# Kernel tuning notes

Hardware: AMD Instinct MI355X
Metric: run time of the kernel (lower is better)

## Reference

```python
import jax, jax.numpy as jnp
import numpy as np

E = 1024  # embed_dim
H = 1     # num_heads (energy_W matmul forces head_dim == embed_dim)
TEMPERATURE = 1.0


def setup_inputs() -> dict:
    key = jax.random.key(0)
    ks = jax.random.split(key, 10)
    B, S = 8, 2048
    inp = {
        "query": jax.random.normal(ks[0], (B, S, E), dtype=jnp.float32),
        "key": jax.random.normal(ks[1], (B, S, E), dtype=jnp.float32),
        "value": jax.random.normal(ks[2], (B, S, E), dtype=jnp.float32),
        "mask": jnp.ones((1, 1, S, S), dtype=jnp.int32),
        # nn.Linear params (y = x @ W.T + b)
        "Wq": jax.random.normal(ks[3], (E, E), dtype=jnp.float32) * (1.0 / np.sqrt(E)),
        "bq": jnp.zeros((E,), dtype=jnp.float32),
        "Wk": jax.random.normal(ks[4], (E, E), dtype=jnp.float32) * (1.0 / np.sqrt(E)),
        "bk": jnp.zeros((E,), dtype=jnp.float32),
        "Wv": jax.random.normal(ks[5], (E, E), dtype=jnp.float32) * (1.0 / np.sqrt(E)),
        "bv": jnp.zeros((E,), dtype=jnp.float32),
        "energy_W": jax.random.normal(ks[6], (E, E), dtype=jnp.float32),
    }
    return inp


def reference(query, key, value, mask, Wq, bq, Wk, bk, Wv, bv, energy_W):
    B, S, _ = query.shape
    hd = E // H
    # projections (torch Linear: x @ W.T + b), then split heads -> [B, H, S, hd]
    q = (query @ Wq.T + bq).reshape(B, S, H, hd).transpose(0, 2, 1, 3)
    k = (key @ Wk.T + bk).reshape(B, S, H, hd).transpose(0, 2, 1, 3)
    v = (value @ Wv.T + bv).reshape(B, S, H, hd).transpose(0, 2, 1, 3)
    # bilinear energy: (q) @ (k @ W)^T   -> [B, H, Sq, Sk]
    k_t = k @ energy_W
    energy = jnp.einsum("bhqd,bhkd->bhqk", q, k_t) / TEMPERATURE
    energy = jnp.where(mask == 0, jnp.float32(-1e9), energy)
    attn_weights = jax.nn.softmax(-energy, axis=-1)
    out = jnp.einsum("bhqk,bhkd->bhqd", attn_weights, v)
    out = out.transpose(0, 2, 1, 3).reshape(B, S, E)
    return (out, attn_weights)
```

## Files before the change

kernel.cpp:

```cpp
#include <hip/hip_runtime.h>


typedef __attribute__((ext_vector_type(8))) short short8;
typedef __attribute__((ext_vector_type(4))) float f32x4;

#define E_DIM 1024
#define S_LEN 2048
#define NB 8

__device__ __forceinline__ unsigned short rne_bf(float x) {
    unsigned int u = __float_as_uint(x);
    return (unsigned short)((u + 0x7fffu + ((u >> 16) & 1u)) >> 16);
}

__device__ __forceinline__ void splitbf(float x, unsigned short& h, unsigned short& l) {
    unsigned int u = __float_as_uint(x);
    unsigned int rh = ((u + 0x7fffu + ((u >> 16) & 1u)) >> 16) << 16;
    h = (unsigned short)(rh >> 16);
    float r = x - __uint_as_float(rh);
    unsigned int v = __float_as_uint(r);
    l = (unsigned short)((v + 0x7fffu + ((v >> 16) & 1u)) >> 16);
}

__device__ __forceinline__ void lds_cp16(const void* g, void* l) {
    __builtin_amdgcn_global_load_lds(
        (const __attribute__((address_space(1))) unsigned int*)g,
        (__attribute__((address_space(3))) unsigned int*)l, 16, 0, 0);
}

__device__ __forceinline__ void wait_vm8() { asm volatile("s_waitcnt vmcnt(8)" ::: "memory"); }
__device__ __forceinline__ void wait_vm4() { asm volatile("s_waitcnt vmcnt(4)" ::: "memory"); }
__device__ __forceinline__ void wait_vm0() { asm volatile("s_waitcnt vmcnt(0)" ::: "memory"); }

template <bool DO_L>
__global__ __launch_bounds__(256) void conv_img(
    const float* __restrict__ src, unsigned short* __restrict__ h,
    unsigned short* __restrict__ l, int ld, int nkt)
{
    const int t = threadIdx.x;
    const long long tb = ((long long)blockIdx.y * nkt + blockIdx.x) * 4096;
    const float* s0 = src + (long long)blockIdx.y * 128 * ld + blockIdx.x * 32;
#pragma unroll
    for (int i = 0; i < 4; ++i) {
        const int f = i * 256 + t;
        const int r = f >> 3;
        const int c4 = (f & 7) << 2;
        const float4 v = *(const float4*)(s0 + (long long)r * ld + c4);
        const int gg = c4 >> 3;
        const int half = (c4 >> 2) & 1;
        const long long wo = tb + (long long)(gg * 128 + r) * 8 + half * 4;
        unsigned short h0, h1, h2, h3;
        if (DO_L) {
            unsigned short l0, l1, l2, l3;
            splitbf(v.x, h0, l0); splitbf(v.y, h1, l1);
            splitbf(v.z, h2, l2); splitbf(v.w, h3, l3);
            uint2 hp, lp;
            hp.x = h0 | ((unsigned)h1 << 16); hp.y = h2 | ((unsigned)h3 << 16);
            lp.x = l0 | ((unsigned)l1 << 16); lp.y = l2 | ((unsigned)l3 << 16);
            *(uint2*)(h + wo) = hp;
            *(uint2*)(l + wo) = lp;
        } else {
            h0 = rne_bf(v.x); h1 = rne_bf(v.y); h2 = rne_bf(v.z); h3 = rne_bf(v.w);
            uint2 hp;
            hp.x = h0 | ((unsigned)h1 << 16); hp.y = h2 | ((unsigned)h3 << 16);
            *(uint2*)(h + wo) = hp;
        }
    }
}

template <int NPROD, int WMODE>
__global__ __launch_bounds__(256) void gemm_img(
    const unsigned short* __restrict__ Ah, const unsigned short* __restrict__ Al,
    const unsigned short* __restrict__ Bh, const unsigned short* __restrict__ Bl,
    float* __restrict__ C, const float* __restrict__ bias,
    unsigned short* __restrict__ imgH, unsigned short* __restrict__ imgL,
    int ldC, long long bsC, int nkt, int aZrb, int bZrb, int outNkt)
{
    extern __shared__ unsigned short sm[];

    const int t = threadIdx.x;
    const int wv = t >> 6, lane = t & 63;
    const int wm = (wv >> 1) << 6, wn = (wv & 1) << 6;
    const int lr = lane & 15, gq = lane >> 4;

    int bx = blockIdx.x, by = blockIdx.y;
    {
        const int gx = gridDim.x, nwg = gx * gridDim.y;
        if ((nwg & 7) == 0) {
            const int w = by * gx + bx;
            const int cpx = nwg >> 3;
            const int sw = (w & 7) * cpx + (w >> 3);
            bx = sw % gx;
            by = sw / gx;
        }
    }

    const long long aB0 = ((long long)blockIdx.z * aZrb + by) * nkt * 4096;
    const long long bB0 = ((long long)blockIdx.z * bZrb + bx) * nkt * 4096;

    auto srcptr = [&](int s, const unsigned short*& aS, const unsigned short*& bS) {
        int seg, kt;
        if (NPROD == 3) {
            seg = (s >= 2 * nkt) ? 2 : (s >= nkt ? 1 : 0);
            kt = s - seg * nkt;
        } else { seg = 0; kt = s; }
        aS = ((NPROD == 3 && seg == 1) ? Al : Ah) + aB0 + (long long)kt * 4096;
        bS = ((NPROD == 3 && seg == 2) ? Bl : Bh) + bB0 + (long long)kt * 4096;
    };
    auto stage = [&](const unsigned short* aS, const unsigned short* bS, int c) {
        unsigned short* dA = sm + c * 8192;
        unsigned short* dB = dA + 4096;
#pragma unroll
        for (int j = 0; j < 2; ++j) {
            lds_cp16(aS + (wv * 128 + j * 64 + lane) * 8, dA + (wv * 128 + j * 64) * 8);
            lds_cp16(bS + (wv * 128 + j * 64 + lane) * 8, dB + (wv * 128 + j * 64) * 8);
        }
    };

    f32x4 acc[4][4] = {};
    const int nsteps = NPROD * nkt;

    {
        const unsigned short *aS, *bS;
        srcptr(0, aS, bS); stage(aS, bS, 0);
        srcptr(1, aS, bS); stage(aS, bS, 1);
    }

    int cur = 0;
    for (int s = 0; s < nsteps; ++s) {
        __builtin_amdgcn_s_barrier();
        if (s + 2 < nsteps) {
            const unsigned short *aS, *bS;
            srcptr(s + 2, aS, bS);
            stage(aS, bS, (cur + 2) % 3);
        }
        if (s + 2 < nsteps) wait_vm8();
        else if (s + 1 < nsteps) wait_vm4();
        else wait_vm0();
        __builtin_amdgcn_s_barrier();
        __builtin_amdgcn_sched_barrier(0);

        const unsigned short* smA = sm + cur * 8192;
        const unsigned short* smB = smA + 4096;
        short8 af[4], bfr[4];
        const unsigned short* pa = smA + (gq * 128 + wm + lr) * 8;
        const unsigned short* pb = smB + (gq * 128 + wn + lr) * 8;
#pragma unroll
        for (int m = 0; m < 4; ++m) af[m] = *(const short8*)(pa + m * 128);
#pragma unroll
        for (int n = 0; n < 4; ++n) bfr[n] = *(const short8*)(pb + n * 128);
        __builtin_amdgcn_s_setprio(1);
#pragma unroll
        for (int m = 0; m < 4; ++m)
#pragma unroll
            for (int n = 0; n < 4; ++n)
                acc[m][n] = __builtin_amdgcn_mfma_f32_16x16x32_bf16(af[m], bfr[n], acc[m][n], 0, 0, 0);
        __builtin_amdgcn_s_setprio(0);
        cur = (cur + 1) % 3;
    }

    const int cr = (lane >> 4) << 2, cc = lane & 15;
    if (WMODE == 0) {
        float* Cb = C + (long long)blockIdx.z * bsC;
#pragma unroll
        for (int m = 0; m < 4; ++m)
#pragma unroll
            for (int n = 0; n < 4; ++n) {
                const int gc = bx * 128 + wn + n * 16 + cc;
                const float badd = bias ? bias[gc] : 0.0f;
                const int gr0 = by * 128 + wm + m * 16 + cr;
#pragma unroll
                for (int i = 0; i < 4; ++i)
                    Cb[(long long)(gr0 + i) * ldC + gc] = acc[m][n][i] + badd;
            }
    } else {
        float* slab = (float*)sm;
        const int wmi = wv >> 1;
#pragma unroll
        for (int m = 0; m < 4; ++m) {
            __syncthreads();
#pragma unroll
            for (int n = 0; n < 4; ++n) {
                const int col = wn + n * 16 + cc;
                const float badd = bias ? bias[bx * 128 + col] : 0.0f;
#pragma unroll
                for (int i = 0; i < 4; ++i)
                    slab[(wmi * 16 + cr + i) * 132 + col] = acc[m][n][i] + badd;
            }
            __syncthreads();
            if (WMODE == 1) {
#pragma unroll
                for (int it = 0; it < 2; ++it) {
                    const int e = it * 256 + t;
                    const int wq = e >> 8, cg = (e >> 4) & 15, fr = e & 15;
                    const float* sp = slab + (wq * 16 + fr) * 132 + cg * 8;
                    const int rIn = wq * 64 + m * 16 + fr;
                    const int ktO = bx * 4 + (cg >> 2);
                    const int gO = cg & 3;
                    const long long base =
                        ((long long)by * outNkt + ktO) * 4096 + (gO * 128 + rIn) * 8;
                    unsigned short h[8], l[8];
#pragma unroll
                    for (int j = 0; j < 8; ++j) splitbf(sp[j], h[j], l[j]);
                    uint4 hp, lp;
                    hp.x = h[0] | ((unsigned)h[1] << 16); hp.y = h[2] | ((unsigned)h[3] << 16);
                    hp.z = h[4] | ((unsigned)h[5] << 16); hp.w = h[6] | ((unsigned)h[7] << 16);
                    lp.x = l[0] | ((unsigned)l[1] << 16); lp.y = l[2] | ((unsigned)l[3] << 16);
                    lp.z = l[4] | ((unsigned)l[5] << 16); lp.w = l[6] | ((unsigned)l[7] << 16);
                    *(uint4*)(imgH + base) = hp;
                    *(uint4*)(imgL + base) = lp;
                }
            } else {
#pragma unroll
                for (int it = 0; it < 2; ++it) {
                    const int e = it * 256 + t;
                    const int wq = e >> 8, s8 = (e >> 7) & 1, dl = e & 127;
                    const int sG = by * 128 + wq * 64 + m * 16 + s8 * 8;
                    const int z = sG >> 11, sIn = sG & 2047;
                    const int ktO = sIn >> 5, gO = (sIn >> 3) & 3;
                    const long long base =
                        ((long long)(z * 8 + bx) * 64 + ktO) * 4096 + (gO * 128 + dl) * 8;
                    unsigned short h[8];
#pragma unroll
                    for (int j = 0; j < 8; ++j)
                        h[j] = rne_bf(slab[(wq * 16 + s8 * 8 + j) * 132 + dl]);
                    uint4 hp;
                    hp.x = h[0] | ((unsigned)h[1] << 16); hp.y = h[2] | ((unsigned)h[3] << 16);
                    hp.z = h[4] | ((unsigned)h[5] << 16); hp.w = h[6] | ((unsigned)h[7] << 16);
                    *(uint4*)(imgH + base) = hp;
                }
            }
        }
    }
}

__global__ __launch_bounds__(256) void softmax_img(
    float* __restrict__ attn, const int* __restrict__ mask,
    unsigned short* __restrict__ img)
{
    const int row = blockIdx.x;
    const int q = row & (S_LEN - 1);
    const int t = threadIdx.x;
    const int lane = t & 63, wid = t >> 6;
    float* rp = attn + (long long)row * S_LEN;
    const int* mp = mask + (long long)q * S_LEN;

    const float4 e0 = *(const float4*)(rp + t * 8);
    const float4 e1 = *(const float4*)(rp + t * 8 + 4);
    const int4 ma = *(const int4*)(mp + t * 8);
    const int4 mb = *(const int4*)(mp + t * 8 + 4);
    float zv[8];
    zv[0] = ma.x ? -e0.x : 1e9f;
    zv[1] = ma.y ? -e0.y : 1e9f;
    zv[2] = ma.z ? -e0.z : 1e9f;
    zv[3] = ma.w ? -e0.w : 1e9f;
    zv[4] = mb.x ? -e1.x : 1e9f;
    zv[5] = mb.y ? -e1.y : 1e9f;
    zv[6] = mb.z ? -e1.z : 1e9f;
    zv[7] = mb.w ? -e1.w : 1e9f;
    float mx = zv[0];
#pragma unroll
    for (int j = 1; j < 8; ++j) mx = fmaxf(mx, zv[j]);
#pragma unroll
    for (int o = 32; o > 0; o >>= 1) mx = fmaxf(mx, __shfl_xor(mx, o));
    __shared__ float redm[4], reds[4];
    if (lane == 0) redm[wid] = mx;
    __syncthreads();
    mx = fmaxf(fmaxf(redm[0], redm[1]), fmaxf(redm[2], redm[3]));
    float s = 0.f;
#pragma unroll
    for (int j = 0; j < 8; ++j) { zv[j] = expf(zv[j] - mx); s += zv[j]; }
#pragma unroll
    for (int o = 32; o > 0; o >>= 1) s += __shfl_xor(s, o);
    if (lane == 0) reds[wid] = s;
    __syncthreads();
    s = reds[0] + reds[1] + reds[2] + reds[3];
    const float inv = 1.0f / s;
    float4 o0, o1;
    o0.x = zv[0] * inv; o0.y = zv[1] * inv; o0.z = zv[2] * inv; o0.w = zv[3] * inv;
    o1.x = zv[4] * inv; o1.y = zv[5] * inv; o1.z = zv[6] * inv; o1.w = zv[7] * inv;
    *(float4*)(rp + t * 8) = o0;
    *(float4*)(rp + t * 8 + 4) = o1;
    const int z = row >> 11, rb = (row >> 7) & 15;
    const int ktO = t >> 2, gO = t & 3, r = row & 127;
    const long long base = (((long long)(z * 16 + rb) * 64 + ktO) * 512 + gO * 128 + r) * 8;
    uint4 hp;
    hp.x = rne_bf(o0.x) | ((unsigned)rne_bf(o0.y) << 16);
    hp.y = rne_bf(o0.z) | ((unsigned)rne_bf(o0.w) << 16);
    hp.z = rne_bf(o1.x) | ((unsigned)rne_bf(o1.y) << 16);
    hp.w = rne_bf(o1.z) | ((unsigned)rne_bf(o1.w) << 16);
    *(uint4*)(img + base) = hp;
}

__global__ void transpose1024(const float* __restrict__ in, float* __restrict__ out)
{
    __shared__ float tile[32][33];
    const int bx = blockIdx.x << 5, by = blockIdx.y << 5;
    const int tx = threadIdx.x, ty = threadIdx.y;
#pragma unroll
    for (int i = 0; i < 4; ++i)
        tile[ty + 8 * i][tx] = in[(long long)(by + ty + 8 * i) * E_DIM + bx + tx];
    __syncthreads();
#pragma unroll
    for (int i = 0; i < 4; ++i)
        out[(long long)(bx + ty + 8 * i) * E_DIM + by + tx] = tile[tx][ty + 8 * i];
}

__global__ __launch_bounds__(256) void bias_c_kernel(
    const float* __restrict__ We, const float* __restrict__ bq, float* __restrict__ c)
{
    const int i = blockIdx.x;
    const int t = threadIdx.x;
    float s = 0.f;
    for (int d = t; d < E_DIM; d += 256) s += bq[d] * We[(long long)i * E_DIM + d];
#pragma unroll
    for (int o = 32; o > 0; o >>= 1) s += __shfl_xor(s, o);
    __shared__ float red[4];
    if ((t & 63) == 0) red[t >> 6] = s;
    __syncthreads();
    if (t == 0) c[i] = red[0] + red[1] + red[2] + red[3];
}

template <bool SPLIT, int WMODE>
__global__ __launch_bounds__(256) void gemm_split(
    const float* __restrict__ A, const float* __restrict__ B,
    float* __restrict__ C, const float* __restrict__ bias,
    int M, int N, int K,
    long long bsA, long long bsB, long long bsC)
{
    extern __shared__ unsigned short sm[];
    unsigned short* sAh = sm;
    unsigned short* sBh = sm + 5120;
    unsigned short* sAl = sm + 10240;
    unsigned short* sBl = sm + 15360;

    const int t = threadIdx.x;
    const int z = blockIdx.z;
    const float* Ab = A + (long long)z * bsA + (long long)blockIdx.y * 128 * K;
    const float* Bb = B + (long long)z * bsB + (long long)blockIdx.x * 128 * K;

    const int wv = t >> 6;
    const int lane = t & 63;
    const int wm = (wv >> 1) << 6;
    const int wn = (wv & 1) << 6;
    const int lr = lane & 15;
    const int ko = (lane >> 4) << 3;

    f32x4 acc[4][4] = {};

    for (int k0 = 0; k0 < K; k0 += 32) {
        __syncthreads();
#pragma unroll
        for (int i = 0; i < 4; ++i) {
            const int f = t + (i << 8);
            const int row = f >> 3;
            const int c4 = (f & 7) << 2;
            const float4 av = *(const float4*)(Ab + (long long)row * K + k0 + c4);
            const float4 bv = *(const float4*)(Bb + (long long)row * K + k0 + c4);
            if (SPLIT) {
                unsigned short h0, h1, h2, h3, l0, l1, l2, l3;
                splitbf(av.x, h0, l0); splitbf(av.y, h1, l1);
                splitbf(av.z, h2, l2); splitbf(av.w, h3, l3);
                uint2 hp, lp;
                hp.x = (unsigned)h0 | ((unsigned)h1 << 16);
                hp.y = (unsigned)h2 | ((unsigned)h3 << 16);
                lp.x = (unsigned)l0 | ((unsigned)l1 << 16);
                lp.y = (unsigned)l2 | ((unsigned)l3 << 16);
                *(uint2*)(sAh + row * 40 + c4) = hp;
                *(uint2*)(sAl + row * 40 + c4) = lp;
                splitbf(bv.x, h0, l0); splitbf(bv.y, h1, l1);
                splitbf(bv.z, h2, l2); splitbf(bv.w, h3, l3);
                hp.x = (unsigned)h0 | ((unsigned)h1 << 16);
                hp.y = (unsigned)h2 | ((unsigned)h3 << 16);
                lp.x = (unsigned)l0 | ((unsigned)l1 << 16);
                lp.y = (unsigned)l2 | ((unsigned)l3 << 16);
                *(uint2*)(sBh + row * 40 + c4) = hp;
                *(uint2*)(sBl + row * 40 + c4) = lp;
            } else {
                uint2 hp;
                hp.x = (unsigned)rne_bf(av.x) | ((unsigned)rne_bf(av.y) << 16);
                hp.y = (unsigned)rne_bf(av.z) | ((unsigned)rne_bf(av.w) << 16);
                *(uint2*)(sAh + row * 40 + c4) = hp;
                hp.x = (unsigned)rne_bf(bv.x) | ((unsigned)rne_bf(bv.y) << 16);
                hp.y = (unsigned)rne_bf(bv.z) | ((unsigned)rne_bf(bv.w) << 16);
                *(uint2*)(sBh + row * 40 + c4) = hp;
            }
        }
        __syncthreads();
        short8 ah[4], bh[4], al[4], bl[4];
#pragma unroll
        for (int m = 0; m < 4; ++m)
            ah[m] = *(const short8*)(sAh + (wm + m * 16 + lr) * 40 + ko);
#pragma unroll
        for (int n = 0; n < 4; ++n)
            bh[n] = *(const short8*)(sBh + (wn + n * 16 + lr) * 40 + ko);
        if (SPLIT) {
#pragma unroll
            for (int m = 0; m < 4; ++m)
                al[m] = *(const short8*)(sAl + (wm + m * 16 + lr) * 40 + ko);
#pragma unroll
            for (int n = 0; n < 4; ++n)
                bl[n] = *(const short8*)(sBl + (wn + n * 16 + lr) * 40 + ko);
        }
#pragma unroll
        for (int m = 0; m < 4; ++m) {
#pragma unroll
            for (int n = 0; n < 4; ++n) {
                acc[m][n] = __builtin_amdgcn_mfma_f32_16x16x32_bf16(ah[m], bh[n], acc[m][n], 0, 0, 0);
                if (SPLIT) {
                    acc[m][n] = __builtin_amdgcn_mfma_f32_16x16x32_bf16(ah[m], bl[n], acc[m][n], 0, 0, 0);
                    acc[m][n] = __builtin_amdgcn_mfma_f32_16x16x32_bf16(al[m], bh[n], acc[m][n], 0, 0, 0);
                }
            }
        }
    }

    const int cr = (lane >> 4) << 2;
    const int cc = lane & 15;
    float* Cb = C + (long long)z * bsC;
#pragma unroll
    for (int m = 0; m < 4; ++m) {
#pragma unroll
        for (int n = 0; n < 4; ++n) {
            const int gc = blockIdx.x * 128 + wn + n * 16 + cc;
            const float badd = bias ? bias[gc] : 0.0f;
            const int gr0 = blockIdx.y * 128 + wm + m * 16 + cr;
#pragma unroll
            for (int i = 0; i < 4; ++i) {
                const float val = acc[m][n][i] + badd;
                if (WMODE == 0) {
                    Cb[(long long)(gr0 + i) * N + gc] = val;
                } else {
                    const int r = gr0 + i;
                    Cb[(long long)(r >> 11) * ((long long)N * 2048) +
                       (long long)gc * 2048 + (r & 2047)] = val;
                }
            }
        }
    }
}

__global__ __launch_bounds__(256) void softmax_rows(
    float* __restrict__ attn, const int* __restrict__ mask)
{
    const int row = blockIdx.x;
    const int q = row & (S_LEN - 1);
    const int t = threadIdx.x;
    const int lane = t & 63, wid = t >> 6;
    float* rp = attn + (long long)row * S_LEN;
    const int* mp = mask + (long long)q * S_LEN;

    float zv[8];
    float mx = -3.4e38f;
#pragma unroll
    for (int j = 0; j < 8; ++j) {
        const int idx = t + (j << 8);
        const float e = rp[idx];
        const int mv = mp[idx];
        const float zz = (mv != 0) ? -e : 1e9f;
        zv[j] = zz;
        mx = fmaxf(mx, zz);
    }
#pragma unroll
    for (int o = 32; o > 0; o >>= 1) mx = fmaxf(mx, __shfl_xor(mx, o));
    __shared__ float redm[4], reds[4];
    if (lane == 0) redm[wid] = mx;
    __syncthreads();
    mx = fmaxf(fmaxf(redm[0], redm[1]), fmaxf(redm[2], redm[3]));

    float s = 0.f;
#pragma unroll
    for (int j = 0; j < 8; ++j) { zv[j] = expf(zv[j] - mx); s += zv[j]; }
#pragma unroll
    for (int o = 32; o > 0; o >>= 1) s += __shfl_xor(s, o);
    if (lane == 0) reds[wid] = s;
    __syncthreads();
    s = reds[0] + reds[1] + reds[2] + reds[3];
    const float inv = 1.0f / s;
#pragma unroll
    for (int j = 0; j < 8; ++j) rp[t + (j << 8)] = zv[j] * inv;
}

extern "C" void kernel_launch(void* const* d_in, const int* in_sizes, int n_in,
                              void* d_out, int out_size, void* d_ws, size_t ws_size,
                              hipStream_t stream)
{
    const float* query = (const float*)d_in[0];
    const float* key   = (const float*)d_in[1];
    const float* value = (const float*)d_in[2];
    const int*   mask  = (const int*)d_in[3];
    const float* Wq    = (const float*)d_in[4];
    const float* bq    = (const float*)d_in[5];
    const float* Wk    = (const float*)d_in[6];
    const float* bk    = (const float*)d_in[7];
    const float* Wv    = (const float*)d_in[8];
    const float* bv    = (const float*)d_in[9];
    const float* We    = (const float*)d_in[10];

    float* out  = (float*)d_out;
    float* attn = out + (long long)NB * S_LEN * E_DIM;

    const size_t oWqT  = 0;
    const size_t oCvec = oWqT + (4u << 20);
    const size_t oWqTH = oCvec + 4096;
    const size_t oWqTL = oWqTH + (2u << 20);
    const size_t oWeH  = oWqTL + (2u << 20);
    const size_t oWeL  = oWeH + (2u << 20);
    const size_t oWkH  = oWeL + (2u << 20);
    const size_t oWkL  = oWkH + (2u << 20);
    const size_t oWvH  = oWkL + (2u << 20);
    const size_t oPH   = oWvH + (2u << 20);
    const size_t oPL   = oPH + (2u << 20);
    const size_t oBig1 = oPL + (2u << 20);
    const size_t oBig2 = oBig1 + (64u << 20);
    const size_t oBig3 = oBig2 + (64u << 20);
    const size_t NEED  = oBig3 + (64u << 20);

    char* wsb = (char*)d_ws;

    if (ws_size >= NEED) {
        float* WqT  = (float*)(wsb + oWqT);
        float* cvec = (float*)(wsb + oCvec);
        unsigned short* WqTH = (unsigned short*)(wsb + oWqTH);
        unsigned short* WqTL = (unsigned short*)(wsb + oWqTL);
        unsigned short* WeH  = (unsigned short*)(wsb + oWeH);
        unsigned short* WeL  = (unsigned short*)(wsb + oWeL);
        unsigned short* WkH  = (unsigned short*)(wsb + oWkH);
        unsigned short* WkL  = (unsigned short*)(wsb + oWkL);
        unsigned short* WvH  = (unsigned short*)(wsb + oWvH);
        unsigned short* PH   = (unsigned short*)(wsb + oPH);
        unsigned short* PL   = (unsigned short*)(wsb + oPL);
        unsigned short* qryH = (unsigned short*)(wsb + oBig1);
        unsigned short* qryL = (unsigned short*)(wsb + oBig1 + (32u << 20));
        unsigned short* attnH = (unsigned short*)(wsb + oBig1);
        unsigned short* keyH = (unsigned short*)(wsb + oBig2);
        unsigned short* keyL = (unsigned short*)(wsb + oBig2 + (32u << 20));
        unsigned short* qwH  = (unsigned short*)(wsb + oBig2);
        unsigned short* qwL  = (unsigned short*)(wsb + oBig2 + (32u << 20));
        unsigned short* kH   = (unsigned short*)(wsb + oBig3);
        unsigned short* kL   = (unsigned short*)(wsb + oBig3 + (32u << 20));
        unsigned short* vTH  = (unsigned short*)(wsb + oBig3);
        unsigned short* valH = (unsigned short*)(wsb + oBig3 + (32u << 20));

        transpose1024<<<dim3(32, 32), dim3(32, 8), 0, stream>>>(Wq, WqT);
        bias_c_kernel<<<1024, 256, 0, stream>>>(We, bq, cvec);
        conv_img<true><<<dim3(32, 8), 256, 0, stream>>>(WqT, WqTH, WqTL, 1024, 32);
        conv_img<true><<<dim3(32, 8), 256, 0, stream>>>(We, WeH, WeL, 1024, 32);
        conv_img<true><<<dim3(32, 8), 256, 0, stream>>>(Wk, WkH, WkL, 1024, 32);
        conv_img<false><<<dim3(32, 8), 256, 0, stream>>>(Wv, WvH, nullptr, 1024, 32);
        conv_img<true><<<dim3(32, 128), 256, 0, stream>>>(query, qryH, qryL, 1024, 32);
        conv_img<true><<<dim3(32, 128), 256, 0, stream>>>(key, keyH, keyL, 1024, 32);

        gemm_img<3, 1><<<dim3(8, 8, 1), 256, 49152, stream>>>(
            WeH, WeL, WqTH, WqTL, nullptr, nullptr, PH, PL, 0, 0, 32, 0, 0, 32);
        gemm_img<3, 1><<<dim3(8, 128, 1), 256, 49152, stream>>>(
            keyH, keyL, WkH, WkL, nullptr, bk, kH, kL, 0, 0, 32, 0, 0, 32);
        gemm_img<3, 1><<<dim3(8, 128, 1), 256, 49152, stream>>>(
            qryH, qryL, PH, PL, nullptr, cvec, qwH, qwL, 0, 0, 32, 0, 0, 32);
        gemm_img<3, 0><<<dim3(16, 16, NB), 256, 49152, stream>>>(
            qwH, qwL, kH, kL, attn, nullptr, nullptr, nullptr,
            2048, (long long)S_LEN * S_LEN, 32, 16, 16, 0);
        conv_img<false><<<dim3(32, 128), 256, 0, stream>>>(value, valH, nullptr, 1024, 32);
        gemm_img<1, 3><<<dim3(8, 128, 1), 256, 49152, stream>>>(
            valH, nullptr, WvH, nullptr, nullptr, bv, vTH, nullptr, 0, 0, 32, 0, 0, 0);
        softmax_img<<<NB * S_LEN, 256, 0, stream>>>(attn, mask, attnH);
        gemm_img<1, 0><<<dim3(8, 16, NB), 256, 49152, stream>>>(
            attnH, nullptr, vTH, nullptr, out, nullptr, nullptr, nullptr,
            1024, (long long)S_LEN * E_DIM, 64, 16, 8, 0);
    } else {
        float* ws   = (float*)d_ws;
        float* WqT  = ws;
        float* P    = WqT + 1048576;
        float* cvec = P + 1048576;
        float* kbuf = cvec + 1024;
        float* qw   = kbuf + 16777216;
        float* vT   = qw + 16777216;
        const size_t need_old = (size_t)(1048576 * 2 + 1024 + 16777216 * 3) * 4;
        if (ws_size < need_old) return;

        transpose1024<<<dim3(32, 32), dim3(32, 8), 0, stream>>>(Wq, WqT);
        bias_c_kernel<<<1024, 256, 0, stream>>>(We, bq, cvec);
        gemm_split<true, 0><<<dim3(8, 8, 1), 256, 40960, stream>>>(
            We, WqT, P, nullptr, 1024, 1024, 1024, 0, 0, 0);
        gemm_split<true, 0><<<dim3(8, 128, 1), 256, 40960, stream>>>(
            key, Wk, kbuf, bk, 16384, 1024, 1024, 0, 0, 0);
        gemm_split<false, 1><<<dim3(8, 128, 1), 256, 20480, stream>>>(
            value, Wv, vT, bv, 16384, 1024, 1024, 0, 0, 0);
        gemm_split<true, 0><<<dim3(8, 128, 1), 256, 40960, stream>>>(
            query, P, qw, cvec, 16384, 1024, 1024, 0, 0, 0);
        gemm_split<true, 0><<<dim3(16, 16, NB), 256, 40960, stream>>>(
            qw, kbuf, attn, nullptr, 2048, 2048, 1024,
            (long long)S_LEN * E_DIM, (long long)S_LEN * E_DIM, (long long)S_LEN * S_LEN);
        softmax_rows<<<NB * S_LEN, 256, 0, stream>>>(attn, mask);
        gemm_split<false, 0><<<dim3(8, 16, NB), 256, 20480, stream>>>(
            attn, vT, out, nullptr, 2048, 1024, 2048,
            (long long)S_LEN * S_LEN, (long long)E_DIM * S_LEN, (long long)S_LEN * E_DIM);
    }

    (void)in_sizes; (void)n_in; (void)out_size;
}
```

Baseline: 824.3 us.

## Add 256x128-tile 512-thread GEMM kernel for energy and output matmuls

Introduces gemm_big, a 512-thread kernel that computes a 256x128 output tile per block with a three-stage LDS ring buffered by direct global-to-LDS loads, and uses it for the QK^T energy GEMM and the attention-times-V GEMM. It also replaces the block remapping with a swizzle that groups blocks into 4x4 chunks per XCD to improve L2 reuse, applied to the existing GEMMs too. The larger tile halves the A/B refetch per output and the deeper pipeline aims to hide load latency. The cost is more registers and LDS per block, which may reduce occupancy.

```diff
diff --git a/kernel.cpp b/kernel.cpp
--- a/kernel.cpp
+++ b/kernel.cpp
@@ -29,8 +29,30 @@
 }
 
 __device__ __forceinline__ void wait_vm8() { asm volatile("s_waitcnt vmcnt(8)" ::: "memory"); }
+__device__ __forceinline__ void wait_vm6() { asm volatile("s_waitcnt vmcnt(6)" ::: "memory"); }
 __device__ __forceinline__ void wait_vm4() { asm volatile("s_waitcnt vmcnt(4)" ::: "memory"); }
+__device__ __forceinline__ void wait_vm3() { asm volatile("s_waitcnt vmcnt(3)" ::: "memory"); }
 __device__ __forceinline__ void wait_vm0() { asm volatile("s_waitcnt vmcnt(0)" ::: "memory"); }
+
+__device__ __forceinline__ void swizzle_xy(int& bx, int& by) {
+    const int gx = gridDim.x, gy = gridDim.y;
+    const int nwg = gx * gy;
+    const int w = by * gx + bx;
+    if ((gx & 3) == 0 && (gy & 3) == 0 && (((gx >> 2) * (gy >> 2)) & 7) == 0) {
+        const int nchx = gx >> 2;
+        const int xcd = w & 7, i = w >> 3;
+        const int j = i >> 4, p = i & 15;
+        const int ch = xcd + 8 * j;
+        const int chy = ch / nchx, chx = ch - chy * nchx;
+        by = chy * 4 + (p >> 2);
+        bx = chx * 4 + (p & 3);
+    } else if ((nwg & 7) == 0) {
+        const int cpx = nwg >> 3;
+        const int sw = (w & 7) * cpx + (w >> 3);
+        bx = sw % gx;
+        by = sw / gx;
+    }
+}
 
 template <bool DO_L>
 __global__ __launch_bounds__(256) void conv_img(
@@ -68,6 +90,109 @@
     }
 }
 
+template <int NPROD>
+__global__ __launch_bounds__(512, 4) void gemm_big(
+    const unsigned short* __restrict__ Ah, const unsigned short* __restrict__ Al,
+    const unsigned short* __restrict__ Bh, const unsigned short* __restrict__ Bl,
+    float* __restrict__ C, const float* __restrict__ bias,
+    int ldC, long long bsC, int nkt, int aZrb, int bZrb)
+{
+    __shared__ unsigned short smb[36864];
+
+    const int t = threadIdx.x;
+    const int wv = t >> 6, lane = t & 63;
+    const int wr = wv >> 1, wc = wv & 1;
+    const int lr = lane & 15, gq = lane >> 4;
+
+    int bx = blockIdx.x, by = blockIdx.y;
+    swizzle_xy(bx, by);
+
+    const long long aB0 = ((long long)blockIdx.z * aZrb + 2 * by) * nkt * 4096;
+    const long long aB1 = aB0 + (long long)nkt * 4096;
+    const long long bB0 = ((long long)blockIdx.z * bZrb + bx) * nkt * 4096;
+
+    auto srcptr = [&](int s, const unsigned short*& a0, const unsigned short*& a1,
+                      const unsigned short*& bS) {
+        int seg, kt;
+        if (NPROD == 3) {
+            seg = (s >= 2 * nkt) ? 2 : (s >= nkt ? 1 : 0);
+            kt = s - seg * nkt;
+        } else { seg = 0; kt = s; }
+        const unsigned short* aBase = ((NPROD == 3 && seg == 1) ? Al : Ah);
+        const unsigned short* bBase = ((NPROD == 3 && seg == 2) ? Bl : Bh);
+        a0 = aBase + aB0 + (long long)kt * 4096;
+        a1 = aBase + aB1 + (long long)kt * 4096;
+        bS = bBase + bB0 + (long long)kt * 4096;
+    };
+    auto stage = [&](const unsigned short* a0, const unsigned short* a1,
+                     const unsigned short* bS, int c) {
+        unsigned short* dA = smb + c * 12288;
+        lds_cp16(a0 + t * 8, dA + t * 8);
+        lds_cp16(a1 + t * 8, dA + 4096 + t * 8);
+        lds_cp16(bS + t * 8, dA + 8192 + t * 8);
+    };
+
+    f32x4 acc[4][4] = {};
+    const int nsteps = NPROD * nkt;
+
+    {
+        const unsigned short *a0, *a1, *bS;
+        srcptr(0, a0, a1, bS); stage(a0, a1, bS, 0);
+        srcptr(1, a0, a1, bS); stage(a0, a1, bS, 1);
+    }
+
+    int cur = 0;
+    for (int s = 0; s < nsteps; ++s) {
+        __builtin_amdgcn_s_barrier();
+        if (s + 2 < nsteps) {
+            const unsigned short *a0, *a1, *bS;
+            srcptr(s + 2, a0, a1, bS);
+            stage(a0, a1, bS, (cur + 2) % 3);
+        }
+        if (s + 2 < nsteps) wait_vm6();
+        else if (s + 1 < nsteps) wait_vm3();
+        else wait_vm0();
+        __builtin_amdgcn_s_barrier();
+        __builtin_amdgcn_sched_barrier(0);
+
+        const unsigned short* dA = smb + cur * 12288;
+        const unsigned short* dB = dA + 8192;
+        short8 af[4], bfr[4];
+#pragma unroll
+        for (int m = 0; m < 4; ++m) {
+            const int R = wr * 64 + m * 16 + lr;
+            af[m] = *(const short8*)(dA + (R >> 7) * 4096 + (gq * 128 + (R & 127)) * 8);
+        }
+#pragma unroll
+        for (int n = 0; n < 4; ++n) {
+            const int Cc = wc * 64 + n * 16 + lr;
+            bfr[n] = *(const short8*)(dB + (gq * 128 + Cc) * 8);
+        }
+        __builtin_amdgcn_s_setprio(1);
+#pragma unroll
+        for (int m = 0; m < 4; ++m)
+#pragma unroll
+            for (int n = 0; n < 4; ++n)
+                acc[m][n] = __builtin_amdgcn_mfma_f32_16x16x32_bf16(af[m], bfr[n], acc[m][n], 0, 0, 0);
+        __builtin_amdgcn_s_setprio(0);
+        cur = (cur + 1) % 3;
+    }
+
+    const int cr = (lane >> 4) << 2, cc = lane & 15;
+    float* Cb = C + (long long)blockIdx.z * bsC;
+#pragma unroll
+    for (int m = 0; m < 4; ++m)
+#pragma unroll
+        for (int n = 0; n < 4; ++n) {
+            const int gc = bx * 128 + wc * 64 + n * 16 + cc;
+            const float badd = bias ? bias[gc] : 0.0f;
+            const int gr0 = by * 256 + wr * 64 + m * 16 + cr;
+#pragma unroll
+            for (int i = 0; i < 4; ++i)
+                Cb[(long long)(gr0 + i) * ldC + gc] = acc[m][n][i] + badd;
+        }
+}
+
 template <int NPROD, int WMODE>
 __global__ __launch_bounds__(256) void gemm_img(
     const unsigned short* __restrict__ Ah, const unsigned short* __restrict__ Al,
@@ -84,16 +209,7 @@
     const int lr = lane & 15, gq = lane >> 4;
 
     int bx = blockIdx.x, by = blockIdx.y;
-    {
-        const int gx = gridDim.x, nwg = gx * gridDim.y;
-        if ((nwg & 7) == 0) {
-            const int w = by * gx + bx;
-            const int cpx = nwg >> 3;
-            const int sw = (w & 7) * cpx + (w >> 3);
-            bx = sw % gx;
-            by = sw / gx;
-        }
-    }
+    swizzle_xy(bx, by);
 
     const long long aB0 = ((long long)blockIdx.z * aZrb + by) * nkt * 4096;
     const long long bB0 = ((long long)blockIdx.z * bZrb + bx) * nkt * 4096;
@@ -557,16 +673,16 @@
             keyH, keyL, WkH, WkL, nullptr, bk, kH, kL, 0, 0, 32, 0, 0, 32);
         gemm_img<3, 1><<<dim3(8, 128, 1), 256, 49152, stream>>>(
             qryH, qryL, PH, PL, nullptr, cvec, qwH, qwL, 0, 0, 32, 0, 0, 32);
-        gemm_img<3, 0><<<dim3(16, 16, NB), 256, 49152, stream>>>(
-            qwH, qwL, kH, kL, attn, nullptr, nullptr, nullptr,
-            2048, (long long)S_LEN * S_LEN, 32, 16, 16, 0);
+        gemm_big<3><<<dim3(16, 8, NB), 512, 0, stream>>>(
+            qwH, qwL, kH, kL, attn, nullptr,
+            2048, (long long)S_LEN * S_LEN, 32, 16, 16);
         conv_img<false><<<dim3(32, 128), 256, 0, stream>>>(value, valH, nullptr, 1024, 32);
         gemm_img<1, 3><<<dim3(8, 128, 1), 256, 49152, stream>>>(
             valH, nullptr, WvH, nullptr, nullptr, bv, vTH, nullptr, 0, 0, 32, 0, 0, 0);
         softmax_img<<<NB * S_LEN, 256, 0, stream>>>(attn, mask, attnH);
-        gemm_img<1, 0><<<dim3(8, 16, NB), 256, 49152, stream>>>(
-            attnH, nullptr, vTH, nullptr, out, nullptr, nullptr, nullptr,
-            1024, (long long)S_LEN * E_DIM, 64, 16, 8, 0);
+        gemm_big<1><<<dim3(8, 8, NB), 512, 0, stream>>>(
+            attnH, nullptr, vTH, nullptr, out, nullptr,
+            1024, (long long)S_LEN * E_DIM, 64, 16, 8);
     } else {
         float* ws   = (float*)d_ws;
         float* WqT  = ws;
```

New measurement: 797.4 us. 3.3% less time.
